# Kernel tuning notes

Measured on AMD Instinct MI355X. Metric: run time of the kernel, lower is better.

Reference implementation:

```python
import jax, jax.numpy as jnp
import numpy as np

VOCAB, HIDDEN, LAYERS = 128, 1024, 2
B, T = 128, 512


def setup_inputs() -> dict:
    key = jax.random.key(0)
    ks = jax.random.split(key, 8)
    s0 = 1.0 / np.sqrt(HIDDEN)
    x = jax.random.normal(ks[0], (B, T, VOCAB), dtype=jnp.float32)
    h = jnp.zeros((LAYERS, B, HIDDEN), dtype=jnp.float32)
    c = jnp.zeros((LAYERS, B, HIDDEN), dtype=jnp.float32)
    # LSTM params, gate order (i, f, g, o) concatenated along last dim (4H)
    Wx0 = jax.random.uniform(ks[1], (VOCAB, 4 * HIDDEN), jnp.float32, -s0, s0)
    Wh0 = jax.random.uniform(ks[2], (HIDDEN, 4 * HIDDEN), jnp.float32, -s0, s0)
    b0 = jax.random.uniform(ks[3], (4 * HIDDEN,), jnp.float32, -s0, s0)
    Wx1 = jax.random.uniform(ks[4], (HIDDEN, 4 * HIDDEN), jnp.float32, -s0, s0)
    Wh1 = jax.random.uniform(ks[5], (HIDDEN, 4 * HIDDEN), jnp.float32, -s0, s0)
    b1 = jax.random.uniform(ks[6], (4 * HIDDEN,), jnp.float32, -s0, s0)
    return {"x": x, "h": h, "c": c, "Wx0": Wx0, "Wh0": Wh0, "b0": b0,
            "Wx1": Wx1, "Wh1": Wh1, "b1": b1}


def _lstm_cell(inp, h_prev, c_prev, Wx, Wh, b):
    gates = inp @ Wx + h_prev @ Wh + b            # (B, 4H)
    i, f, g, o = jnp.split(gates, 4, axis=-1)
    i = jax.nn.sigmoid(i)
    f = jax.nn.sigmoid(f)
    g = jnp.tanh(g)
    o = jax.nn.sigmoid(o)
    c_new = f * c_prev + i * g
    h_new = o * jnp.tanh(c_new)
    return h_new, c_new


def reference(x, h, c, Wx0, Wh0, b0, Wx1, Wh1, b1):
    layer_params = [(Wx0, Wh0, b0), (Wx1, Wh1, b1)]

    def step(carry, x_t):
        h_prev, c_prev = carry                    # each (L, B, H)
        inp = x_t                                 # (B, VOCAB)
        hs, cs = [], []
        for l, (Wx, Wh, b) in enumerate(layer_params):
            h_new, c_new = _lstm_cell(inp, h_prev[l], c_prev[l], Wx, Wh, b)
            hs.append(h_new)
            cs.append(c_new)
            inp = h_new
        return (jnp.stack(hs), jnp.stack(cs)), hs[-1]

    xs = jnp.swapaxes(x, 0, 1)                    # (T, B, VOCAB)
    (h_f, c_f), outs = jax.lax.scan(step, (h, c), xs)
    outs = jnp.swapaxes(outs, 0, 1)               # (B, T, H)
    return outs, h_f, c_f
```

## Files before the change

### kernel.cpp

```cpp
#include <hip/hip_runtime.h>

#define VV 128
#define HH 1024
#define BB 128
#define TT 512
#define G4 4096
#define BTH ((size_t)BB * TT * HH)
#define HPAR (4 * 64 * 512)
#define RING 32

typedef __attribute__((ext_vector_type(8))) short bf16x8;
typedef __attribute__((ext_vector_type(16))) float f32x16;

__device__ __forceinline__ short f2bf(float f) {
  unsigned u = __float_as_uint(f);
  u = (u + 0x7fffu + ((u >> 16) & 1u)) >> 16;
  return (short)u;
}

__device__ __forceinline__ float fsig(float x) {
  x = fminf(fmaxf(x, -30.f), 30.f);
  float e = __expf(-x);
  return 1.f / (1.f + e);
}
__device__ __forceinline__ float ftanh(float x) {
  x = fminf(fmaxf(x, -15.f), 15.f);
  float e = __expf(-2.f * x);
  return (1.f - e) / (1.f + e);
}

__device__ __forceinline__ unsigned eidx(int t) {
  return ((unsigned)(t + 1) * 37u) & (RING - 1);
}


__global__ void init_state(const float* __restrict__ h,
                           short* __restrict__ h0dst, short* __restrict__ h1dst) {
  const int n = 2 * HPAR;
  for (int i = blockIdx.x * blockDim.x + threadIdx.x; i < n; i += gridDim.x * blockDim.x) {
    int inner = i & (HPAR - 1);
    int l = i >> 17;
    int e = i & 7, lane = (i >> 3) & 63, kc = (i >> 9) & 63, rb = (i >> 15) & 3;
    int row = rb * 32 + (lane & 31);
    int j = kc * 16 + ((lane >> 5) << 3) + e;
    short hb = f2bf(h[((size_t)l * BB + row) * HH + j]);
    (l ? h1dst : h0dst)[inner] = hb;
  }
}

__global__ void pack_w(const float* __restrict__ Wx0, const float* __restrict__ Wh0,
                       const float* __restrict__ Wx1, const float* __restrict__ Wh1,
                       short* __restrict__ wp0, short* __restrict__ wp1) {
  const int n0 = 128 * 72 * 512;
  const int n1 = 128 * 128 * 512;
  for (int i = blockIdx.x * blockDim.x + threadIdx.x; i < n0 + n1; i += gridDim.x * blockDim.x) {
    if (i < n0) {
      int cu = i / (72 * 512);
      int rem = i - cu * (72 * 512);
      int kc = rem >> 9, le = rem & 511;
      int lane = le >> 3, e = le & 7;
      int k = kc * 16 + ((lane >> 5) << 3) + e;
      int cl = lane & 31;
      int gcol = (cl >> 3) * HH + cu * 8 + (cl & 7);
      float f = (k < VV) ? Wx0[(size_t)k * G4 + gcol] : Wh0[(size_t)(k - VV) * G4 + gcol];
      wp0[i] = f2bf(f);
    } else {
      int j = i - n0;
      int cu = j >> 16;
      int rem = j & 65535;
      int kc = rem >> 9, le = rem & 511;
      int lane = le >> 3, e = le & 7;
      int k = kc * 16 + ((lane >> 5) << 3) + e;
      int cl = lane & 31;
      int gcol = (cl >> 3) * HH + cu * 8 + (cl & 7);
      float f = (k < HH) ? Wx1[(size_t)k * G4 + gcol] : Wh1[(size_t)(k - HH) * G4 + gcol];
      wp1[j] = f2bf(f);
    }
  }
}

__global__ void pack_b(const float* __restrict__ b0, const float* __restrict__ b1,
                       float* __restrict__ bp, unsigned* __restrict__ slots) {
  int i = blockIdx.x * blockDim.x + threadIdx.x;
  if (i < 2 * 128 * 32) {
    int l = i >> 12;
    int cu = (i >> 5) & 127;
    int cc = i & 31;
    const float* b = l ? b1 : b0;
    bp[i] = b[(cc >> 3) * HH + cu * 8 + (cc & 7)];
  }
  if (i < 512) slots[i] = 0u;
}


template <int NCH>
__device__ __forceinline__ void hgemm(f32x16* acc, const short* pa0, const short* pa1,
                                      const short* __restrict__ pb) {
  constexpr int NG = NCH / 16;
  bf16x8 A[3][16];
#pragma unroll
  for (int g = 0; g < 3; ++g) {
#pragma unroll
    for (int j = 0; j < 16; ++j) {
      const int c = g * 16 + j;
      const short* ap = (c < 64) ? (pa0 + c * 512) : (pa1 + (c - 64) * 512);
      asm volatile("global_load_dwordx4 %0, %1, off" : "=v"(A[g][j]) : "v"(ap));
    }
  }
#pragma unroll
  for (int g = 0; g < NG; ++g) {
    const int rem = NG - 1 - g;
    if (rem >= 2)      asm volatile("s_waitcnt vmcnt(32)" ::: "memory");
    else if (rem == 1) asm volatile("s_waitcnt vmcnt(16)" ::: "memory");
    else               asm volatile("s_waitcnt vmcnt(0)" ::: "memory");
#pragma unroll
    for (int j = 0; j < 16; ++j)
      asm volatile("" : "+v"(A[g % 3][j]));
#pragma unroll
    for (int j = 0; j < 16; ++j) {
      const int c = g * 16 + j;
      bf16x8 b = *(const bf16x8*)(pb + c * 512);
      acc[j & 3] = __builtin_amdgcn_mfma_f32_32x32x16_bf16(A[g % 3][j], b, acc[j & 3], 0, 0, 0);
    }
    if (g + 3 < NG) {
#pragma unroll
      for (int j = 0; j < 16; ++j) {
        const int c = (g + 3) * 16 + j;
        const short* ap = (c < 64) ? (pa0 + c * 512) : (pa1 + (c - 64) * 512);
        asm volatile("global_load_dwordx4 %0, %1, off"
                     : "=v"(A[(g + 3) % 3][j]) : "v"(ap));
      }
    }
  }
}

__device__ __forceinline__ void xgemm_raw(f32x16* acc, const float* __restrict__ xlane,
                                          const short* __restrict__ pb) {
#pragma unroll
  for (int c = 0; c < 8; ++c) {
    float4 lo = *(const float4*)(xlane + c * 16);
    float4 hi = *(const float4*)(xlane + c * 16 + 4);
    bf16x8 a;
    a[0] = f2bf(lo.x); a[1] = f2bf(lo.y); a[2] = f2bf(lo.z); a[3] = f2bf(lo.w);
    a[4] = f2bf(hi.x); a[5] = f2bf(hi.y); a[6] = f2bf(hi.z); a[7] = f2bf(hi.w);
    bf16x8 b = *(const bf16x8*)(pb + c * 512);
    acc[c & 3] = __builtin_amdgcn_mfma_f32_32x32x16_bf16(a, b, acc[c & 3], 0, 0, 0);
  }
}

__global__ void __launch_bounds__(256, 1) lstm_main(const float* __restrict__ x,
    short* __restrict__ h0b, short* __restrict__ h1b,
    const short* __restrict__ wp0, const short* __restrict__ wp1,
    const float* __restrict__ bpack, const float* __restrict__ cin,
    float* __restrict__ out, unsigned* __restrict__ slots) {
  __shared__ short wlds[128 * 512];
  __shared__ short hstage[4][256];
  unsigned* gdone = slots + 256;
  const int blk = blockIdx.x;
  const int layer = blk >> 7;
  const int cu = blk & 127;
  const int tid = threadIdx.x;
  const int lane = tid & 63;
  const int wave = tid >> 6;
  const bool isRelay = ((blk & 15) == 0) && (blk < 128);
  const int rbase = (blk >> 4) << 5;

  const int nkc = layer ? 128 : 72;
  const short* wsrc = layer ? (wp1 + (size_t)cu * 128 * 512) : (wp0 + (size_t)cu * 72 * 512);
  for (int i = tid; i < nkc * 64; i += 256)
    ((int4*)wlds)[i] = ((const int4*)wsrc)[i];
  __syncthreads();

  const int col = lane & 31;
  const float bias = bpack[layer * 4096 + cu * 32 + col];
  const int uu = col & 7;
  const bool ewlane = (col < 8);
  const int gcol = cu * 8 + uu;
  const int hi4 = ((lane >> 5) << 2);
  const int arow = wave * 32 + col;
  const int koff = (lane >> 5) << 3;
  const float* xlane0 = x + (size_t)arow * (TT * VV) + koff;

  float creg[16], hval[16];
#pragma unroll
  for (int r = 0; r < 16; ++r) {
    int grow = wave * 32 + (r & 3) + ((r >> 2) << 3) + hi4;
    creg[r] = ewlane ? cin[(size_t)layer * BB * HH + (size_t)grow * HH + gcol] : 0.f;
    hval[r] = 0.f;
  }

  const int pst = (wave * 64 + (cu >> 1)) * 512 + ((cu & 1) << 8);
  const int wv64 = wave * 64 * 512 + lane * 8;

  f32x16 acc[4];
  auto initacc = [&]() {
#pragma unroll
    for (int r = 0; r < 16; ++r) {
      acc[0][r] = bias; acc[1][r] = 0.f; acc[2][r] = 0.f; acc[3][r] = 0.f;
    }
  };

  if (layer == 0) {
    initacc();
    xgemm_raw(acc, xlane0, wlds + lane * 8);
  }

  for (int p = 0; p <= TT; ++p) {
    if (p > 0) {
      const unsigned tgt = (unsigned)p;
      if (isRelay && tid < 32) {
        for (;;) {
          unsigned v = __hip_atomic_load(&slots[rbase + tid],
                                         __ATOMIC_RELAXED, __HIP_MEMORY_SCOPE_AGENT);
          if (__all(v >= tgt)) break;
        }
        if (tid == 0)
          __hip_atomic_store(&gdone[(blk >> 4) << 5], tgt,
                             __ATOMIC_RELAXED, __HIP_MEMORY_SCOPE_AGENT);
      }
      if (tid < 8) {
        for (;;) {
          unsigned v = __hip_atomic_load(&gdone[tid << 5],
                                         __ATOMIC_RELAXED, __HIP_MEMORY_SCOPE_AGENT);
          if (__all(v >= tgt)) break;
          __builtin_amdgcn_s_sleep(1);
        }
      }
      __syncthreads();
    }

    const bool active = layer ? (p >= 1) : (p < TT);
    const int t = layer ? (p - 1) : p;
    if (active) {
      const short* ra0 = h0b + (size_t)eidx(p - 1) * HPAR + wv64;
      const short* ra1 = h1b + (size_t)eidx(p - 2) * HPAR + wv64;
      if (layer == 0) {
        hgemm<64>(acc, ra0, ra0, wlds + 8 * 512 + lane * 8);
      } else {
        initacc();
        hgemm<128>(acc, ra0, ra1, wlds + lane * 8);
      }
      f32x16 accf = (acc[0] + acc[1]) + (acc[2] + acc[3]);
#pragma unroll
      for (int r = 0; r < 16; ++r) {
        float a0 = accf[r];
        float nl = (col >= 16 && col < 24) ? ftanh(a0) : fsig(a0);
        float f_ = __shfl_xor(nl, 8);
        float g_ = __shfl_xor(nl, 16);
        float o_ = __shfl_xor(nl, 24);
        const int rloc = (r & 3) + ((r >> 2) << 3) + hi4;
        const int grow = wave * 32 + rloc;
        float hnew = 0.f;
        if (ewlane) {
          float cnew = f_ * creg[r] + nl * g_;
          creg[r] = cnew;
          hnew = o_ * ftanh(cnew);
          hval[r] = hnew;
          hstage[wave][rloc * 8 + uu] = f2bf(hnew);
          if (t == TT - 1) {
            out[BTH + (size_t)layer * BB * HH + (size_t)grow * HH + gcol] = hnew;
            out[BTH + (size_t)(2 + layer) * BB * HH + (size_t)grow * HH + gcol] = creg[r];
          }
        }
      }
      if (p < TT) {
        short* hp = (layer ? h1b + (size_t)eidx(p - 1) * HPAR
                           : h0b + (size_t)eidx(p) * HPAR) + pst;
        if (lane < 32) {
          bf16x8 v = *(const bf16x8*)&hstage[wave][lane * 8];
          asm volatile("global_store_dwordx4 %0, %1, off sc0 sc1"
                       :: "v"(hp + lane * 8), "v"(v) : "memory");
        }
        asm volatile("s_waitcnt vmcnt(0)" ::: "memory");
      }
    }

    if (p == TT) {
      if (layer && active && ewlane) {
#pragma unroll
        for (int r = 0; r < 16; ++r) {
          const int rloc = (r & 3) + ((r >> 2) << 3) + hi4;
          const int grow = wave * 32 + rloc;
          out[(size_t)grow * TT * HH + (size_t)t * HH + gcol] = hval[r];
        }
      }
      break;
    }

    __syncthreads();
    if (tid == 0)
      __hip_atomic_store(&slots[blk], (unsigned)(p + 1),
                         __ATOMIC_RELAXED, __HIP_MEMORY_SCOPE_AGENT);

    if (layer == 0) {
      if (p + 1 < TT) {
        initacc();
        xgemm_raw(acc, xlane0 + (size_t)(p + 1) * VV, wlds + lane * 8);
      }
    } else if (active && ewlane) {
#pragma unroll
      for (int r = 0; r < 16; ++r) {
        const int rloc = (r & 3) + ((r >> 2) << 3) + hi4;
        const int grow = wave * 32 + rloc;
        out[(size_t)grow * TT * HH + (size_t)t * HH + gcol] = hval[r];
      }
    }
  }
}


extern "C" void kernel_launch(void* const* d_in, const int* in_sizes, int n_in,
                              void* d_out, int out_size, void* d_ws, size_t ws_size,
                              hipStream_t stream) {
  const float* x   = (const float*)d_in[0];
  const float* h   = (const float*)d_in[1];
  const float* c   = (const float*)d_in[2];
  const float* Wx0 = (const float*)d_in[3];
  const float* Wh0 = (const float*)d_in[4];
  const float* b0  = (const float*)d_in[5];
  const float* Wx1 = (const float*)d_in[6];
  const float* Wh1 = (const float*)d_in[7];
  const float* b1  = (const float*)d_in[8];
  float* out = (float*)d_out;

  char* ws = (char*)d_ws;
  short* wp0 = (short*)ws;
  short* wp1 = (short*)(ws + 9437184);
  float* bp  = (float*)(ws + 26214400);
  unsigned* slots = (unsigned*)(ws + 26247168);
  short* h0r = (short*)(ws + 26249216);
  short* h1r = (short*)(ws + 34637824);

  hipLaunchKernelGGL(init_state, dim3(512),  dim3(256), 0, stream, h, h0r, h1r);
  hipLaunchKernelGGL(pack_w,     dim3(4096), dim3(256), 0, stream, Wx0, Wh0, Wx1, Wh1, wp0, wp1);
  hipLaunchKernelGGL(pack_b,     dim3(32),   dim3(256), 0, stream, b0, b1, bp, slots);

  hipLaunchKernelGGL(lstm_main, dim3(256), dim3(256), 0, stream,
                     x, h0r, h1r, wp0, wp1, bp, c, out, slots);
}
```

Before: 6.391 ms.

## Replace two-level relay barrier with direct vectorized flag polling per block

Removes the relay blocks that gathered per-block progress flags and republished them to a global done array. Instead, wave 0 of every block polls all 256 slot counters directly with 16-byte system-coherent loads (sc0 sc1). Layer-0 blocks wait on layer-1 progress only with a 24-step slack, so layer 0 can run ahead of layer 1. This cuts one hop of cross-block latency per timestep but makes every block hammer the same flag cache lines, and it relies on the slot layout matching 4 contiguous counters per lane.

```diff
diff --git a/kernel.cpp b/kernel.cpp
--- a/kernel.cpp
+++ b/kernel.cpp
@@ -11,6 +11,7 @@
 
 typedef __attribute__((ext_vector_type(8))) short bf16x8;
 typedef __attribute__((ext_vector_type(16))) float f32x16;
+typedef __attribute__((ext_vector_type(4))) unsigned u32x4;
 
 __device__ __forceinline__ short f2bf(float f) {
   unsigned u = __float_as_uint(f);
@@ -155,15 +156,12 @@
     float* __restrict__ out, unsigned* __restrict__ slots) {
   __shared__ short wlds[128 * 512];
   __shared__ short hstage[4][256];
-  unsigned* gdone = slots + 256;
   const int blk = blockIdx.x;
   const int layer = blk >> 7;
   const int cu = blk & 127;
   const int tid = threadIdx.x;
   const int lane = tid & 63;
   const int wave = tid >> 6;
-  const bool isRelay = ((blk & 15) == 0) && (blk < 128);
-  const int rbase = (blk >> 4) << 5;
 
   const int nkc = layer ? 128 : 72;
   const short* wsrc = layer ? (wp1 + (size_t)cu * 128 * 512) : (wp0 + (size_t)cu * 72 * 512);
@@ -207,22 +205,18 @@
 
   for (int p = 0; p <= TT; ++p) {
     if (p > 0) {
-      const unsigned tgt = (unsigned)p;
-      if (isRelay && tid < 32) {
+      if (wave == 0) {
+        const unsigned pp = (unsigned)p;
+        unsigned tgt;
+        if (layer) tgt = pp;
+        else       tgt = (lane < 32) ? pp : (p > 24 ? pp - 24u : 0u);
+        const unsigned* p0 = slots + (lane << 2);
         for (;;) {
-          unsigned v = __hip_atomic_load(&slots[rbase + tid],
-                                         __ATOMIC_RELAXED, __HIP_MEMORY_SCOPE_AGENT);
-          if (__all(v >= tgt)) break;
-        }
-        if (tid == 0)
-          __hip_atomic_store(&gdone[(blk >> 4) << 5], tgt,
-                             __ATOMIC_RELAXED, __HIP_MEMORY_SCOPE_AGENT);
-      }
-      if (tid < 8) {
-        for (;;) {
-          unsigned v = __hip_atomic_load(&gdone[tid << 5],
-                                         __ATOMIC_RELAXED, __HIP_MEMORY_SCOPE_AGENT);
-          if (__all(v >= tgt)) break;
+          u32x4 v;
+          asm volatile("global_load_dwordx4 %0, %1, off sc0 sc1\n\ts_waitcnt vmcnt(0)"
+                       : "=v"(v) : "v"(p0) : "memory");
+          bool ok = (v[0] >= tgt) && (v[1] >= tgt) && (v[2] >= tgt) && (v[3] >= tgt);
+          if (__all(ok)) break;
           __builtin_amdgcn_s_sleep(1);
         }
       }
```

After: 6.666 ms. 4.3% more time.
